# Performance work log

Measured on AMD Instinct MI355X. Metric: run time of the kernel, lower is better.

Reference implementation:

```python
import math
import jax, jax.numpy as jnp
import numpy as np

W_SIZE = 7
NUM_HEADS = 12


def _shift_masks(w: int, d: int):
    # upper/lower mask (applied to last row of windows)
    ul = np.zeros((w * w, w * w), np.float32)
    ul[-d * w:, :-d * w] = -np.inf
    ul[:-d * w, -d * w:] = -np.inf
    # left/right mask (applied to last column of windows)
    lr = np.zeros((w, w, w, w), np.float32)
    lr[:, -d:, :, :-d] = -np.inf
    lr[:, :-d, :, -d:] = -np.inf
    lr = lr.reshape(w * w, w * w)
    return jnp.asarray(ul), jnp.asarray(lr)


def _rel_pos_index(w: int):
    # standard Swin relative-position index, shape (w*w, w*w), values in [0, (2w-1)^2)
    coords = np.stack(np.meshgrid(np.arange(w), np.arange(w), indexing='ij'), 0).reshape(2, -1)  # (2, w*w)
    rel = coords[:, :, None] - coords[:, None, :]  # (2, ww, ww)
    idx = (rel[0] + w - 1) * (2 * w - 1) + (rel[1] + w - 1)
    return jnp.asarray(idx, dtype=jnp.int32)


def setup_inputs() -> dict:
    key = jax.random.key(0)
    ks = jax.random.split(key, 6)
    E, w = 384, W_SIZE
    return {
        'x': jax.random.normal(ks[0], (32, 56, 56, E), jnp.float32),
        'w_qkv': jax.random.normal(ks[1], (3 * E, E), jnp.float32) * 0.02,
        'b_qkv': jax.random.normal(ks[2], (3 * E,), jnp.float32) * 0.02,
        'w_proj': jax.random.normal(ks[3], (E, E), jnp.float32) * 0.02,
        'b_proj': jax.random.normal(ks[4], (E,), jnp.float32) * 0.02,
        'rel_table': jax.random.normal(ks[5], ((2 * w - 1) ** 2, NUM_HEADS), jnp.float32) * 0.02,
    }


def reference(x, w_qkv, b_qkv, w_proj, b_proj, rel_table):
    w = W_SIZE
    heads = NUM_HEADS
    B, H, Wd, C = x.shape
    hd = C // heads
    nh, nw, ww = H // w, Wd // w, w * w

    # shift (matches torch roll(shifts=(-w//2, -w//2)) == -4 for w=7)
    x = jnp.roll(x, ((-w) // 2, (-w) // 2), axis=(1, 2))

    # window partition: (B, nh, nw, ww, C)
    xw = x.reshape(B, nh, w, nw, w, C).transpose(0, 1, 3, 2, 4, 5).reshape(B, nh, nw, ww, C)

    qkv = xw @ w_qkv.T + b_qkv  # (B, nh, nw, ww, 3C)
    q, k, v = jnp.split(qkv, 3, axis=-1)

    def heads_first(t):  # (B, nh, nw, heads, ww, hd)
        return t.reshape(B, nh, nw, ww, heads, hd).transpose(0, 1, 2, 4, 3, 5)

    q, k, v = heads_first(q), heads_first(k), heads_first(v)

    attn = jnp.einsum('bhwnqd,bhwnkd->bhwnqk', q, k) * (1.0 / math.sqrt(hd))

    # relative position bias: (heads, ww, ww)
    bias = rel_table[_rel_pos_index(w)].transpose(2, 0, 1)
    attn = attn + bias

    # shift masks on last row / last column of windows
    ul, lr = _shift_masks(w, w // 2)
    mask = jnp.zeros((nh, nw, 1, ww, ww), attn.dtype)
    mask = mask.at[-1].add(ul)
    mask = mask.at[:, -1].add(lr)
    attn = attn + mask

    p = jax.nn.softmax(attn, axis=-1)
    o = jnp.einsum('bhwnqk,bhwnkd->bhwnqd', p, v)  # (B, nh, nw, heads, ww, hd)

    # merge heads and un-window
    o = o.transpose(0, 1, 2, 4, 3, 5).reshape(B, nh, nw, w, w, C)
    o = o.transpose(0, 1, 3, 2, 4, 5).reshape(B, H, Wd, C)

    o = jnp.roll(o, (w // 2, w // 2), axis=(1, 2))
    return o @ w_proj.T + b_proj
```

## Files before the change

### kernel.cpp

```cpp
#include <hip/hip_runtime.h>
#include <hip/hip_bf16.h>


typedef __bf16 bf16x8 __attribute__((ext_vector_type(8)));
typedef float  floatx4 __attribute__((ext_vector_type(4)));
typedef short  short8  __attribute__((ext_vector_type(8)));

#define MFMA16(a, b, c) __builtin_amdgcn_mfma_f32_16x16x32_bf16((a), (b), (c), 0, 0, 0)

static __device__ __forceinline__ void gload_lds16(const void* g, void* l) {
  __builtin_amdgcn_global_load_lds(
      (const __attribute__((address_space(1))) void*)g,
      (__attribute__((address_space(3))) void*)l, 16, 0, 0);
}

static __device__ __forceinline__ int src_off(int gm) {
  int win = gm / 49, t = gm - win * 49;
  int b = win >> 6, rr = win & 63;
  int wi = rr >> 3, wj = rr & 7;
  int ty = t / 7, tx = t - ty * 7;
  int y = wi * 7 + ty + 4; if (y >= 56) y -= 56;
  int x = wj * 7 + tx + 4; if (x >= 56) x -= 56;
  return ((b * 56 + y) * 56 + x) * 384;
}

static __device__ __forceinline__ int dst_off(int gm) {
  int win = gm / 49, t = gm - win * 49;
  int b = win >> 6, rr = win & 63;
  int wi = rr >> 3, wj = rr & 7;
  int ty = t / 7, tx = t - ty * 7;
  int y = wi * 7 + ty + 3; if (y >= 56) y -= 56;
  int x = wj * 7 + tx + 3; if (x >= 56) x -= 56;
  return ((b * 56 + y) * 56 + x) * 384;
}

__global__ __launch_bounds__(256) void prep_kernel(
    const float* __restrict__ w_qkv, const float* __restrict__ w_proj,
    const float* __restrict__ rel_table,
    __hip_bfloat16* __restrict__ wqkv_bf, __hip_bfloat16* __restrict__ wproj_bf,
    __hip_bfloat16* __restrict__ bias2) {
  const int N1 = 3 * 384 * 384;
  const int N2 = 384 * 384;
  const int N3 = 12 * 4 * 4 * 64 * 4;
  int i = blockIdx.x * 256 + threadIdx.x;
  if (i < N1) wqkv_bf[i] = __float2bfloat16(w_qkv[i]);
  int j = i - N1;
  if (j >= 0 && j < N2) wproj_bf[j] = __float2bfloat16(w_proj[j]);
  int k = i - N1 - N2;
  if (k >= 0 && k < N3) {
    int r = k & 3;
    int q1 = k >> 2;
    int lp = q1 & 63;
    int q2 = q1 >> 6;
    int ni = q2 & 3;
    int q3 = q2 >> 2;
    int mi = q3 & 3;
    int head = q3 >> 2;
    int g2 = lp >> 4, qq = lp & 15;
    int m = mi * 16 + g2 * 4 + r, n = ni * 16 + qq;
    float val = 0.f;
    if (m < 49 && n < 49) {
      int dy = m / 7 - n / 7 + 6;
      int dx = m % 7 - n % 7 + 6;
      val = rel_table[(dy * 13 + dx) * 12 + head];
    }
    bias2[k] = __float2bfloat16(val);
  }
}

__global__ __launch_bounds__(256) void xconv_kernel(
    const float* __restrict__ x, __hip_bfloat16* __restrict__ xw) {
  int gid = blockIdx.x * 256 + threadIdx.x;
  int row = gid / 48;
  int c = (gid - row * 48) * 8;
  int so = src_off(row) + c;
  floatx4 a = *(const floatx4*)(x + so);
  floatx4 b = *(const floatx4*)(x + so + 4);
  union { __hip_bfloat16 h[8]; short8 s; } u;
#pragma unroll
  for (int i = 0; i < 4; ++i) {
    u.h[i]     = __float2bfloat16(a[i]);
    u.h[4 + i] = __float2bfloat16(b[i]);
  }
  *(short8*)(xw + (size_t)row * 384 + c) = u.s;
}

__global__ __launch_bounds__(256) void qkv_kernel(
    const __hip_bfloat16* __restrict__ xw, const __hip_bfloat16* __restrict__ wq,
    const float* __restrict__ bqkv,
    __hip_bfloat16* __restrict__ qb, __hip_bfloat16* __restrict__ kb,
    __hip_bfloat16* __restrict__ vt) {
  __shared__ __hip_bfloat16 lds[2 * 16384];
  int blk = blockIdx.x;
  int b2 = (blk & 7) * 882 + (blk >> 3);
  int mt = b2 / 9, nt = b2 - mt * 9;
  int tid = threadIdx.x;
  int l = tid & 63, wv = tid >> 6;
  int wm = wv >> 1, wn = wv & 1;
  int g = l >> 4, q16 = l & 15;

  const bool swapped = (nt >= 6);
  const int aro = (swapped ? wn : wm) * 64;
  const int bro = (swapped ? wm : wn) * 64;

  int sr = tid >> 3;
  int sc = tid & 7;
  int scs = sc ^ (sr & 7);

  const __hip_bfloat16* abase = xw + (size_t)(mt * 128) * 384;
  const __hip_bfloat16* bbase = wq + (size_t)(nt * 128) * 384;

  floatx4 acc[4][4];
#pragma unroll
  for (int i = 0; i < 4; ++i)
#pragma unroll
    for (int j = 0; j < 4; ++j)
#pragma unroll
      for (int r = 0; r < 4; ++r) acc[i][j][r] = 0.f;

  auto stage = [&](int buf, int kt) {
    int k0 = kt * 64;
    __hip_bfloat16* la = lds + buf * 16384;
#pragma unroll
    for (int c = 0; c < 4; ++c) {
      int r = c * 32 + sr;
      gload_lds16(abase + (size_t)r * 384 + k0 + scs * 8, la + c * 2048 + tid * 8);
      gload_lds16(bbase + (size_t)r * 384 + k0 + scs * 8, la + 8192 + c * 2048 + tid * 8);
    }
  };

  auto compute = [&](int buf) {
    const __hip_bfloat16* la = lds + buf * 16384;
    const __hip_bfloat16* lb = la + 8192;
#pragma unroll
    for (int kk = 0; kk < 2; ++kk) {
      bf16x8 af[4], bf[4];
#pragma unroll
      for (int i = 0; i < 4; ++i) {
        int r = aro + i * 16 + q16;
        int cp = (kk * 4 + g) ^ (r & 7);
        af[i] = *(const bf16x8*)(la + r * 64 + cp * 8);
      }
#pragma unroll
      for (int i = 0; i < 4; ++i) {
        int r = bro + i * 16 + q16;
        int cp = (kk * 4 + g) ^ (r & 7);
        bf[i] = *(const bf16x8*)(lb + r * 64 + cp * 8);
      }
      if (!swapped) {
#pragma unroll
        for (int i = 0; i < 4; ++i)
#pragma unroll
          for (int j = 0; j < 4; ++j)
            acc[i][j] = MFMA16(af[i], bf[j], acc[i][j]);
      } else {
#pragma unroll
        for (int i = 0; i < 4; ++i)
#pragma unroll
          for (int j = 0; j < 4; ++j)
            acc[i][j] = MFMA16(bf[i], af[j], acc[i][j]);
      }
    }
  };

  stage(0, 0);
  stage(1, 1);
#pragma unroll
  for (int t = 0; t < 6; ++t) {
    if (t < 5) asm volatile("s_waitcnt vmcnt(8)" ::: "memory");
    else       asm volatile("s_waitcnt vmcnt(0)" ::: "memory");
    __builtin_amdgcn_s_barrier();
    __builtin_amdgcn_sched_barrier(0);
    compute(t & 1);
    if (t < 4) {
      __builtin_amdgcn_s_barrier();
      stage(t & 1, t + 2);
    }
  }

  if (!swapped) {
    const bool isq = (nt < 3);
    __hip_bfloat16* ob2 = isq ? qb : kb;
#pragma unroll
    for (int ni = 0; ni < 4; ++ni) {
      int n = nt * 128 + wn * 64 + ni * 16 + q16;
      float bn = bqkv[n];
      int nn = isq ? n : (n - 384);
#pragma unroll
      for (int mi = 0; mi < 4; ++mi) {
#pragma unroll
        for (int r = 0; r < 4; ++r) {
          int gm = mt * 128 + wm * 64 + mi * 16 + g * 4 + r;
          float v = acc[mi][ni][r] + bn;
          if (isq) v *= 0.17677669529663687f;
          ob2[gm * 384 + nn] = __float2bfloat16(v);
        }
      }
    }
  } else {
    int win4[4], t4[4];
#pragma unroll
    for (int bj = 0; bj < 4; ++bj) {
      int gm = mt * 128 + wn * 64 + bj * 16 + q16;
      int w = gm / 49;
      win4[bj] = w;
      t4[bj] = gm - w * 49;
    }
#pragma unroll
    for (int ai = 0; ai < 4; ++ai) {
#pragma unroll
      for (int r = 0; r < 4; ++r) {
        int n = nt * 128 + wm * 64 + ai * 16 + g * 4 + r;
        float bn = bqkv[n];
        int nnv = n - 768;
#pragma unroll
        for (int bj = 0; bj < 4; ++bj) {
          vt[((size_t)win4[bj] * 384 + nnv) * 64 + t4[bj]] =
              __float2bfloat16(acc[ai][bj][r] + bn);
        }
      }
    }
  }
}

__global__ __launch_bounds__(256) void attnproj_kernel(
    const __hip_bfloat16* __restrict__ qb, const __hip_bfloat16* __restrict__ kb,
    const __hip_bfloat16* __restrict__ vt, const __hip_bfloat16* __restrict__ bias2,
    const __hip_bfloat16* __restrict__ wp, const float* __restrict__ bproj,
    float* __restrict__ out) {
  __shared__ __hip_bfloat16 o_lds[49][392];
  __shared__ __hip_bfloat16 p_lds[4][49][72];
  int blk = blockIdx.x;
  int win = (blk & 7) * 256 + (blk >> 3);
  int tid = threadIdx.x;
  int wv = tid >> 6, l = tid & 63;
  int g = l >> 4, q16 = l & 15;
  int wr = win & 63;
  const bool lastrow = ((wr >> 3) == 7);
  const bool lastcol = ((wr & 7) == 7);

  bf16x8 zf;
#pragma unroll
  for (int i = 0; i < 8; ++i) zf[i] = (__bf16)0.0f;
  floatx4 zc;
  zc[0] = zc[1] = zc[2] = zc[3] = 0.f;

#pragma unroll 1
  for (int hh = 0; hh < 3; ++hh) {
    int head = wv * 3 + hh;
    const __hip_bfloat16* qp = qb + (size_t)(win * 49) * 384 + head * 32 + g * 8;
    const __hip_bfloat16* kp = kb + (size_t)(win * 49) * 384 + head * 32 + g * 8;

    bf16x8 aq[4], bk[4];
#pragma unroll
    for (int mi = 0; mi < 4; ++mi) {
      int row = mi * 16 + q16;
      if (row < 49) {
        aq[mi] = *(const bf16x8*)(qp + row * 384);
        bk[mi] = *(const bf16x8*)(kp + row * 384);
      } else {
        aq[mi] = zf;
        bk[mi] = zf;
      }
    }

    floatx4 s[4][4];
#pragma unroll
    for (int mi = 0; mi < 4; ++mi)
#pragma unroll
      for (int ni = 0; ni < 4; ++ni)
        s[mi][ni] = MFMA16(aq[mi], bk[ni], zc);

    const __hip_bfloat16* b2 = bias2 + (size_t)head * 4096;
    float rsum[4][4];
#pragma unroll
    for (int mi = 0; mi < 4; ++mi) {
      float bb[4][4];
#pragma unroll
      for (int ni = 0; ni < 4; ++ni) {
        const __hip_bfloat16* bp4 = b2 + ((mi * 4 + ni) * 64 + l) * 4;
#pragma unroll
        for (int r = 0; r < 4; ++r) bb[ni][r] = __bfloat162float(bp4[r]);
      }
#pragma unroll
      for (int r = 0; r < 4; ++r) {
        int m = mi * 16 + g * 4 + r;
        int m7 = m % 7;
        float vals[4];
        float mx = -1e30f;
#pragma unroll
        for (int ni = 0; ni < 4; ++ni) {
          int n = ni * 16 + q16;
          float v = -1e30f;
          if (m < 49 && n < 49) {
            v = s[mi][ni][r] + bb[ni][r];
            bool mk = (lastrow && ((m >= 28) != (n >= 28))) ||
                      (lastcol && ((m7 >= 4) != ((n % 7) >= 4)));
            if (mk) v = -1e30f;
          }
          vals[ni] = v;
          mx = fmaxf(mx, v);
        }
#pragma unroll
        for (int d = 1; d < 16; d <<= 1) mx = fmaxf(mx, __shfl_xor(mx, d));
        float sum = 0.f;
#pragma unroll
        for (int ni = 0; ni < 4; ++ni) {
          int n = ni * 16 + q16;
          float p = __expf(vals[ni] - mx);
          if (m >= 49 || n >= 49) p = 0.f;
          sum += p;
          if (m < 49) p_lds[wv][m][n] = __float2bfloat16(p);
        }
#pragma unroll
        for (int d = 1; d < 16; d <<= 1) sum += __shfl_xor(sum, d);
        rsum[mi][r] = sum;
      }
    }

    const __hip_bfloat16* vp = vt + ((size_t)win * 384 + head * 32) * 64;
    floatx4 o[4][2];
#pragma unroll
    for (int mi = 0; mi < 4; ++mi)
#pragma unroll
      for (int n2 = 0; n2 < 2; ++n2) o[mi][n2] = zc;
#pragma unroll
    for (int ks = 0; ks < 2; ++ks) {
      bf16x8 av[4], bv[2];
#pragma unroll
      for (int mi = 0; mi < 4; ++mi) {
        int row = mi * 16 + q16;
        row = row < 49 ? row : 48;
        av[mi] = *(const bf16x8*)&p_lds[wv][row][ks * 32 + g * 8];
      }
#pragma unroll
      for (int n2 = 0; n2 < 2; ++n2)
        bv[n2] = *(const bf16x8*)(vp + (n2 * 16 + q16) * 64 + ks * 32 + g * 8);
#pragma unroll
      for (int mi = 0; mi < 4; ++mi)
#pragma unroll
        for (int n2 = 0; n2 < 2; ++n2)
          o[mi][n2] = MFMA16(av[mi], bv[n2], o[mi][n2]);
    }

#pragma unroll
    for (int mi = 0; mi < 4; ++mi) {
#pragma unroll
      for (int r = 0; r < 4; ++r) {
        int m = mi * 16 + g * 4 + r;
        if (m < 49) {
          float inv = 1.0f / rsum[mi][r];
#pragma unroll
          for (int n2 = 0; n2 < 2; ++n2)
            o_lds[m][head * 32 + n2 * 16 + q16] =
                __float2bfloat16(o[mi][n2][r] * inv);
        }
      }
    }
  }

  __syncthreads();

  floatx4 pacc[4][6];
#pragma unroll
  for (int i = 0; i < 4; ++i)
#pragma unroll
    for (int j = 0; j < 6; ++j)
#pragma unroll
      for (int r = 0; r < 4; ++r) pacc[i][j][r] = 0.f;

  for (int k0 = 0; k0 < 384; k0 += 32) {
    bf16x8 af[4], bfr[6];
#pragma unroll
    for (int mi = 0; mi < 4; ++mi) {
      int row = mi * 16 + q16;
      row = row < 49 ? row : 48;
      af[mi] = *(const bf16x8*)&o_lds[row][k0 + g * 8];
    }
#pragma unroll
    for (int ni = 0; ni < 6; ++ni) {
      int brow = wv * 96 + ni * 16 + q16;
      bfr[ni] = *(const bf16x8*)(wp + (size_t)brow * 384 + k0 + g * 8);
    }
#pragma unroll
    for (int mi = 0; mi < 4; ++mi)
#pragma unroll
      for (int ni = 0; ni < 6; ++ni)
        pacc[mi][ni] = MFMA16(af[mi], bfr[ni], pacc[mi][ni]);
  }

#pragma unroll
  for (int mi = 0; mi < 4; ++mi) {
#pragma unroll
    for (int r = 0; r < 4; ++r) {
      int m = mi * 16 + g * 4 + r;
      if (m < 49) {
        int off = dst_off(win * 49 + m);
#pragma unroll
        for (int ni = 0; ni < 6; ++ni) {
          int n = wv * 96 + ni * 16 + q16;
          out[off + n] = pacc[mi][ni][r] + bproj[n];
        }
      }
    }
  }
}

extern "C" void kernel_launch(void* const* d_in, const int* in_sizes, int n_in,
                              void* d_out, int out_size, void* d_ws, size_t ws_size,
                              hipStream_t stream) {
  const float* x         = (const float*)d_in[0];
  const float* w_qkv     = (const float*)d_in[1];
  const float* b_qkv     = (const float*)d_in[2];
  const float* w_proj    = (const float*)d_in[3];
  const float* b_proj    = (const float*)d_in[4];
  const float* rel_table = (const float*)d_in[5];
  float* out = (float*)d_out;

  char* ws = (char*)d_ws;
  const size_t OFF_WQKV  = 0;
  const size_t OFF_WPROJ = 884736;
  const size_t OFF_BIAS2 = 1179648;
  const size_t OFF_Q     = 1572864;
  const size_t OFF_K     = OFF_Q + 77070336;
  const size_t OFF_VT    = OFF_K + 77070336;

  __hip_bfloat16* wqkv_bf  = (__hip_bfloat16*)(ws + OFF_WQKV);
  __hip_bfloat16* wproj_bf = (__hip_bfloat16*)(ws + OFF_WPROJ);
  __hip_bfloat16* bias2    = (__hip_bfloat16*)(ws + OFF_BIAS2);
  __hip_bfloat16* qb       = (__hip_bfloat16*)(ws + OFF_Q);
  __hip_bfloat16* kb       = (__hip_bfloat16*)(ws + OFF_K);
  __hip_bfloat16* vt       = (__hip_bfloat16*)(ws + OFF_VT);
  __hip_bfloat16* xw       = (__hip_bfloat16*)d_out;


  prep_kernel<<<3072, 256, 0, stream>>>(w_qkv, w_proj, rel_table, wqkv_bf, wproj_bf, bias2);
  xconv_kernel<<<18816, 256, 0, stream>>>(x, xw);
  qkv_kernel<<<7056, 256, 0, stream>>>(xw, wqkv_bf, b_qkv, qb, kb, vt);
  attnproj_kernel<<<2048, 256, 0, stream>>>(qb, kb, vt, bias2, wproj_bf, b_proj, out);
}
```

Before: 419.7 us.

## Restructure attention softmax per 16-row tile, precompute mask bits, raise occupancy

The attention kernel now runs softmax and the P·V MFMA one 16-row tile at a time. This shrinks the probability LDS buffer from 49 rows to 16 rows per wave and drops the full rsum/o register arrays. Mask conditions are computed once into a 64-bit bitmask, and bias values are loaded as packed uint2 and unpacked with bit shifts. V fragments are loaded earlier, before the softmax. Launch bounds now request 3 blocks per SM, and s_setprio wraps the MFMA bursts, trading register headroom for more concurrency. There is no barrier between the p_lds writes and the cross-lane reads within a wave, so correctness depends on wave-synchronous behaviour.

Result: faster. 405.8 us (-3.3%).

```diff
diff --git a/kernel.cpp b/kernel.cpp
--- a/kernel.cpp
+++ b/kernel.cpp
@@ -32,6 +32,13 @@
   int y = wi * 7 + ty + 3; if (y >= 56) y -= 56;
   int x = wj * 7 + tx + 3; if (x >= 56) x -= 56;
   return ((b * 56 + y) * 56 + x) * 384;
+}
+
+static __device__ __forceinline__ float bf_lo(unsigned u) {
+  union { unsigned v; float f; } c; c.v = u << 16; return c.f;
+}
+static __device__ __forceinline__ float bf_hi(unsigned u) {
+  union { unsigned v; float f; } c; c.v = u & 0xFFFF0000u; return c.f;
 }
 
 __global__ __launch_bounds__(256) void prep_kernel(
@@ -223,13 +230,13 @@
   }
 }
 
-__global__ __launch_bounds__(256) void attnproj_kernel(
+__global__ __launch_bounds__(256, 3) void attnproj_kernel(
     const __hip_bfloat16* __restrict__ qb, const __hip_bfloat16* __restrict__ kb,
     const __hip_bfloat16* __restrict__ vt, const __hip_bfloat16* __restrict__ bias2,
     const __hip_bfloat16* __restrict__ wp, const float* __restrict__ bproj,
     float* __restrict__ out) {
   __shared__ __hip_bfloat16 o_lds[49][392];
-  __shared__ __hip_bfloat16 p_lds[4][49][72];
+  __shared__ __hip_bfloat16 p_lds[4][16][72];
   int blk = blockIdx.x;
   int win = (blk & 7) * 256 + (blk >> 3);
   int tid = threadIdx.x;
@@ -239,6 +246,25 @@
   const bool lastrow = ((wr >> 3) == 7);
   const bool lastcol = ((wr & 7) == 7);
 
+  unsigned long long badbits = 0ull;
+#pragma unroll
+  for (int mi = 0; mi < 4; ++mi) {
+#pragma unroll
+    for (int r = 0; r < 4; ++r) {
+      int m = mi * 16 + g * 4 + r;
+      int m7 = m % 7;
+      bool m28 = (m >= 28), m74 = (m7 >= 4);
+#pragma unroll
+      for (int ni = 0; ni < 4; ++ni) {
+        int n = ni * 16 + q16;
+        bool bad = (n >= 49) ||
+                   (lastrow && (m28 != (n >= 28))) ||
+                   (lastcol && (m74 != ((n % 7) >= 4)));
+        if (bad) badbits |= (1ull << ((mi * 4 + r) * 4 + ni));
+      }
+    }
+  }
+
   bf16x8 zf;
 #pragma unroll
   for (int i = 0; i < 8; ++i) zf[i] = (__bf16)0.0f;
@@ -265,39 +291,43 @@
     }
 
     floatx4 s[4][4];
+    __builtin_amdgcn_s_setprio(1);
 #pragma unroll
     for (int mi = 0; mi < 4; ++mi)
 #pragma unroll
       for (int ni = 0; ni < 4; ++ni)
         s[mi][ni] = MFMA16(aq[mi], bk[ni], zc);
+    __builtin_amdgcn_s_setprio(0);
+
+    const __hip_bfloat16* vp = vt + ((size_t)win * 384 + head * 32) * 64;
+    bf16x8 bv[2][2];
+#pragma unroll
+    for (int ks = 0; ks < 2; ++ks)
+#pragma unroll
+      for (int n2 = 0; n2 < 2; ++n2)
+        bv[ks][n2] = *(const bf16x8*)(vp + (n2 * 16 + q16) * 64 + ks * 32 + g * 8);
 
     const __hip_bfloat16* b2 = bias2 + (size_t)head * 4096;
-    float rsum[4][4];
+
 #pragma unroll
     for (int mi = 0; mi < 4; ++mi) {
-      float bb[4][4];
-#pragma unroll
-      for (int ni = 0; ni < 4; ++ni) {
-        const __hip_bfloat16* bp4 = b2 + ((mi * 4 + ni) * 64 + l) * 4;
-#pragma unroll
-        for (int r = 0; r < 4; ++r) bb[ni][r] = __bfloat162float(bp4[r]);
-      }
+      uint2 braw[4];
+#pragma unroll
+      for (int ni = 0; ni < 4; ++ni)
+        braw[ni] = *(const uint2*)(b2 + ((mi * 4 + ni) * 64 + l) * 4);
+
+      float rs[4];
 #pragma unroll
       for (int r = 0; r < 4; ++r) {
         int m = mi * 16 + g * 4 + r;
-        int m7 = m % 7;
         float vals[4];
         float mx = -1e30f;
 #pragma unroll
         for (int ni = 0; ni < 4; ++ni) {
-          int n = ni * 16 + q16;
-          float v = -1e30f;
-          if (m < 49 && n < 49) {
-            v = s[mi][ni][r] + bb[ni][r];
-            bool mk = (lastrow && ((m >= 28) != (n >= 28))) ||
-                      (lastcol && ((m7 >= 4) != ((n % 7) >= 4)));
-            if (mk) v = -1e30f;
-          }
+          float bb = (r == 0) ? bf_lo(braw[ni].x) : (r == 1) ? bf_hi(braw[ni].x)
+                     : (r == 2) ? bf_lo(braw[ni].y) : bf_hi(braw[ni].y);
+          bool bad = (badbits >> ((mi * 4 + r) * 4 + ni)) & 1;
+          float v = bad ? -1e30f : (s[mi][ni][r] + bb);
           vals[ni] = v;
           mx = fmaxf(mx, v);
         }
@@ -306,54 +336,32 @@
         float sum = 0.f;
 #pragma unroll
         for (int ni = 0; ni < 4; ++ni) {
-          int n = ni * 16 + q16;
           float p = __expf(vals[ni] - mx);
-          if (m >= 49 || n >= 49) p = 0.f;
           sum += p;
-          if (m < 49) p_lds[wv][m][n] = __float2bfloat16(p);
+          if (m < 49) p_lds[wv][g * 4 + r][ni * 16 + q16] = __float2bfloat16(p);
         }
 #pragma unroll
         for (int d = 1; d < 16; d <<= 1) sum += __shfl_xor(sum, d);
-        rsum[mi][r] = sum;
-      }
-    }
-
-    const __hip_bfloat16* vp = vt + ((size_t)win * 384 + head * 32) * 64;
-    floatx4 o[4][2];
-#pragma unroll
-    for (int mi = 0; mi < 4; ++mi)
-#pragma unroll
-      for (int n2 = 0; n2 < 2; ++n2) o[mi][n2] = zc;
-#pragma unroll
-    for (int ks = 0; ks < 2; ++ks) {
-      bf16x8 av[4], bv[2];
-#pragma unroll
-      for (int mi = 0; mi < 4; ++mi) {
-        int row = mi * 16 + q16;
-        row = row < 49 ? row : 48;
-        av[mi] = *(const bf16x8*)&p_lds[wv][row][ks * 32 + g * 8];
-      }
-#pragma unroll
-      for (int n2 = 0; n2 < 2; ++n2)
-        bv[n2] = *(const bf16x8*)(vp + (n2 * 16 + q16) * 64 + ks * 32 + g * 8);
-#pragma unroll
-      for (int mi = 0; mi < 4; ++mi)
-#pragma unroll
-        for (int n2 = 0; n2 < 2; ++n2)
-          o[mi][n2] = MFMA16(av[mi], bv[n2], o[mi][n2]);
-    }
-
-#pragma unroll
-    for (int mi = 0; mi < 4; ++mi) {
+        rs[r] = sum;
+      }
+      bf16x8 av0 = *(const bf16x8*)&p_lds[wv][q16][g * 8];
+      bf16x8 av1 = *(const bf16x8*)&p_lds[wv][q16][32 + g * 8];
+      floatx4 o2[2];
+      o2[0] = o2[1] = zc;
+#pragma unroll
+      for (int n2 = 0; n2 < 2; ++n2) {
+        o2[n2] = MFMA16(av0, bv[0][n2], o2[n2]);
+        o2[n2] = MFMA16(av1, bv[1][n2], o2[n2]);
+      }
 #pragma unroll
       for (int r = 0; r < 4; ++r) {
         int m = mi * 16 + g * 4 + r;
         if (m < 49) {
-          float inv = 1.0f / rsum[mi][r];
+          float inv = 1.0f / rs[r];
 #pragma unroll
           for (int n2 = 0; n2 < 2; ++n2)
             o_lds[m][head * 32 + n2 * 16 + q16] =
-                __float2bfloat16(o[mi][n2][r] * inv);
+                __float2bfloat16(o2[n2][r] * inv);
         }
       }
     }
@@ -382,11 +390,13 @@
       int brow = wv * 96 + ni * 16 + q16;
       bfr[ni] = *(const bf16x8*)(wp + (size_t)brow * 384 + k0 + g * 8);
     }
+    __builtin_amdgcn_s_setprio(1);
 #pragma unroll
     for (int mi = 0; mi < 4; ++mi)
 #pragma unroll
       for (int ni = 0; ni < 6; ++ni)
         pacc[mi][ni] = MFMA16(af[mi], bfr[ni], pacc[mi][ni]);
+    __builtin_amdgcn_s_setprio(0);
   }
 
 #pragma unroll
```
